# Kernel tuning notes

Measured on AMD Instinct MI355X. Metric: run time of the kernel, lower is better.

## Reference

```python
import jax, jax.numpy as jnp
import numpy as np

L = 12      # n_layers
C = 768     # n_embd = dim = dim_att
H = 12      # heads
N = 64      # head_size_a
FF = 2688   # dim_ffn = int(768*3.5//32*32)
P = 2       # patch_size
INCH = 4
IMG = 32
NCLS = 1000
FREQ = 256
HC = C // 2  # conv stem channels (dim//2)
B = 32
D_MIX = 32
D_DEC = 64
LNX_EPS = 1e-5 * 8.0 ** 2  # GroupNorm eps with head_size_divisor=8


def _ln(x, w=None, b=None, eps=1e-5):
    m = x.mean(-1, keepdims=True)
    v = x.var(-1, keepdims=True)
    xh = (x - m) * jax.lax.rsqrt(v + eps)
    if w is not None:
        xh = xh * w + b
    return xh


def _shift(x):  # RWKV token shift: prepend zero row, drop last
    return jnp.pad(x, ((0, 0), (1, 0), (0, 0)))[:, :-1]


def _gn_img(x, w, b, groups=32, eps=1e-5):
    Bb, Ch, Hh, Ww = x.shape
    xg = x.reshape(Bb, groups, Ch // groups, Hh, Ww)
    m = xg.mean((2, 3, 4), keepdims=True)
    v = xg.var((2, 3, 4), keepdims=True)
    xg = (xg - m) * jax.lax.rsqrt(v + eps)
    return xg.reshape(Bb, Ch, Hh, Ww) * w[None, :, None, None] + b[None, :, None, None]


def _conv5(x, w, b):
    y = jax.lax.conv_general_dilated(x, w, (1, 1), ((2, 2), (2, 2)),
                                     dimension_numbers=('NCHW', 'OIHW', 'NCHW'))
    return y + b[None, :, None, None]


def _wkv(r, k, v, w, u):
    # r,k,v,w: (B,T,H,N); u: (H,N). S[b,h,i,j]: key i -> value j.
    def step(S, inp):
        rt, kt, vt, wt = inp  # each (B,H,N)
        kv = kt[..., :, None] * vt[..., None, :]           # (B,H,N,N)
        y = jnp.einsum('bhi,bhij->bhj', rt, S + u[None, :, :, None] * kv)
        S = wt[..., :, None] * S + kv
        return S, y
    S0 = jnp.zeros((r.shape[0], H, N, N), r.dtype)
    seq = tuple(jnp.moveaxis(a, 1, 0) for a in (r, k, v, w))
    _, ys = jax.lax.scan(step, S0, seq)
    return jnp.moveaxis(ys, 0, 1)  # (B,T,H,N)


def _timemix(x, p):
    Bb, Tt, _ = x.shape
    xx = _shift(x) - x
    xxx = x + xx * p['maa'][0]
    mix = jnp.tanh(xxx @ p['tm_w1']).reshape(Bb, Tt, 5, D_MIX)
    m = jnp.einsum('btfd,fdc->fbtc', mix, p['tm_w2'])  # (5,B,T,C): mw,mk,mv,mr,mg
    xw = x + xx * (p['maa'][1] + m[0])
    xk = x + xx * (p['maa'][2] + m[1])
    xv = x + xx * (p['maa'][3] + m[2])
    xr = x + xx * (p['maa'][4] + m[3])
    xg = x + xx * (p['maa'][5] + m[4])
    r = (xr @ p['r_w'].T).reshape(Bb, Tt, H, N)
    k = (xk @ p['k_w'].T).reshape(Bb, Tt, H, N)
    v = (xv @ p['v_w'].T).reshape(Bb, Tt, H, N)
    g = jax.nn.silu(xg @ p['g_w'].T)
    ww = p['td'] + jnp.tanh(xw @ p['td_w1']) @ p['td_w2']
    w = jnp.exp(-jnp.exp(ww)).reshape(Bb, Tt, H, N)
    y = _wkv(r, k, v, w, p['faaaa'])  # (B,T,H,N)
    mn = y.mean(-1, keepdims=True)
    vr = y.var(-1, keepdims=True)
    y = ((y - mn) * jax.lax.rsqrt(vr + LNX_EPS)).reshape(Bb, Tt, C) * p['lnx_w'] + p['lnx_b']
    return (y * g) @ p['o_w'].T


def _chanmix(x, p):
    xx = _shift(x) - x
    xk = x + xx * p['fmaa'][0]
    xr = x + xx * p['fmaa'][1]
    k = jnp.square(jax.nn.relu(xk @ p['fk_w'].T))
    return jax.nn.sigmoid(xr @ p['fr_w'].T) * (k @ p['fv_w'].T)


def _forward(x, t, y, c1_w, c1_b, gn1_w, gn1_b, c2_w, c2_b, gn2_w, gn2_b,
             xe_w, xe_b, te_w1, te_b1, te_w2, te_b2, y_tab, ln0_w, ln0_b,
             ln1_w, ln1_b, ln2_w, ln2_b, att_maa, tm_w1, tm_w2, td, td_w1,
             td_w2, faaaa, r_w, k_w, v_w, o_w, g_w, lnx_w, lnx_b, ffn_maa,
             fk_w, fr_w, fv_w, ada_w, ada_b, fl_ada_w, fl_ada_b, fl_w, fl_b):
    Bb = x.shape[0]
    h = jax.nn.silu(_conv5(x, c1_w, c1_b))
    h = _gn_img(h, gn1_w, gn1_b)
    h = jax.nn.silu(_conv5(h, c2_w, c2_b))
    h = _gn_img(h, gn2_w, gn2_b)
    # patchify: (B,HC,IMG,IMG) -> (B,T,P*P*HC)
    G = IMG // P
    h = h.reshape(Bb, HC, G, P, G, P).transpose(0, 2, 4, 1, 3, 5).reshape(Bb, G * G, HC * P * P)
    xs = h @ xe_w.T + xe_b
    # timestep embedding
    half = FREQ // 2
    freqs = jnp.exp(-jnp.log(10000.0) * jnp.arange(half, dtype=jnp.float32) / half)
    ang = t[:, None] * freqs[None]
    temb = jnp.concatenate([jnp.cos(ang), jnp.sin(ang)], -1)
    temb = jax.nn.silu(temb @ te_w1.T + te_b1) @ te_w2.T + te_b2
    c = temb + y_tab[y]  # adaln_input (B,C)
    for l in range(L):
        ada = jax.nn.silu(c) @ ada_w[l].T + ada_b[l]
        sm, scm, gm, sp, scp, gp = jnp.split(ada, 6, axis=1)
        if l == 0:
            xs = _ln(xs, ln0_w, ln0_b)
        p = dict(maa=att_maa[l], tm_w1=tm_w1[l], tm_w2=tm_w2[l], td=td[l],
                 td_w1=td_w1[l], td_w2=td_w2[l], faaaa=faaaa[l], r_w=r_w[l],
                 k_w=k_w[l], v_w=v_w[l], o_w=o_w[l], g_w=g_w[l], lnx_w=lnx_w[l],
                 lnx_b=lnx_b[l], fmaa=ffn_maa[l], fk_w=fk_w[l], fr_w=fr_w[l],
                 fv_w=fv_w[l])
        hmod = _ln(xs, ln1_w[l], ln1_b[l]) * (1 + scm[:, None, :]) + sm[:, None, :]
        xs = xs + gm[:, None, :] * _timemix(hmod, p)
        hmod = _ln(xs, ln2_w[l], ln2_b[l]) * (1 + scp[:, None, :]) + sp[:, None, :]
        xs = xs + gp[:, None, :] * _chanmix(hmod, p)
    ada = jax.nn.silu(c) @ fl_ada_w.T + fl_ada_b
    sh, sc = jnp.split(ada, 2, axis=1)
    out = (_ln(xs, eps=1e-6) * (1 + sc[:, None, :]) + sh[:, None, :]) @ fl_w.T + fl_b
    G = IMG // P
    out = out.reshape(Bb, G, G, P, P, INCH)
    out = jnp.einsum('nhwpqc->nchpwq', out).reshape(Bb, INCH, IMG, IMG)
    return out


def setup_inputs() -> dict:
    key = jax.random.key(0)
    ks = iter(jax.random.split(key, 64))
    def rn(shape, s=0.02):
        return (jax.random.normal(next(ks), shape) * s).astype(jnp.float32)
    inp = {}
    inp['x'] = jax.random.normal(next(ks), (B, INCH, IMG, IMG), jnp.float32)
    inp['t'] = jax.random.uniform(next(ks), (B,), jnp.float32) * 1000.0
    inp['y'] = jax.random.randint(next(ks), (B,), 0, NCLS)
    inp['c1_w'] = rn((HC, INCH, 5, 5), 0.05); inp['c1_b'] = jnp.zeros(HC)
    inp['gn1_w'] = jnp.ones(HC); inp['gn1_b'] = jnp.zeros(HC)
    inp['c2_w'] = rn((HC, HC, 5, 5), 0.02); inp['c2_b'] = jnp.zeros(HC)
    inp['gn2_w'] = jnp.ones(HC); inp['gn2_b'] = jnp.zeros(HC)
    inp['xe_w'] = rn((C, P * P * HC)); inp['xe_b'] = jnp.zeros(C)
    inp['te_w1'] = rn((C, FREQ)); inp['te_b1'] = jnp.zeros(C)
    inp['te_w2'] = rn((C, C)); inp['te_b2'] = jnp.zeros(C)
    inp['y_tab'] = rn((NCLS + 1, C))
    inp['ln0_w'] = jnp.ones(C); inp['ln0_b'] = jnp.zeros(C)
    inp['ln1_w'] = jnp.ones((L, C)); inp['ln1_b'] = jnp.zeros((L, C))
    inp['ln2_w'] = jnp.ones((L, C)); inp['ln2_b'] = jnp.zeros((L, C))
    inp['att_maa'] = jax.random.uniform(next(ks), (L, 6, C), jnp.float32)
    inp['tm_w1'] = rn((L, C, 5 * D_MIX), 0.01)
    inp['tm_w2'] = rn((L, 5, D_MIX, C), 0.01)
    inp['td'] = rn((L, C), 0.5) - 3.0
    inp['td_w1'] = rn((L, C, D_DEC), 0.01)
    inp['td_w2'] = rn((L, D_DEC, C), 0.01)
    inp['faaaa'] = rn((L, H, N), 0.1)
    for nm in ('r_w', 'k_w', 'v_w', 'o_w', 'g_w'):
        inp[nm] = rn((L, C, C))
    inp['lnx_w'] = jnp.ones((L, C)); inp['lnx_b'] = jnp.zeros((L, C))
    inp['ffn_maa'] = jax.random.uniform(next(ks), (L, 2, C), jnp.float32)
    inp['fk_w'] = rn((L, FF, C)); inp['fr_w'] = rn((L, C, C)); inp['fv_w'] = rn((L, C, FF))
    inp['ada_w'] = rn((L, 6 * C, C)); inp['ada_b'] = jnp.zeros((L, 6 * C))
    inp['fl_ada_w'] = rn((2 * C, C)); inp['fl_ada_b'] = jnp.zeros(2 * C)
    inp['fl_w'] = rn((P * P * INCH, C)); inp['fl_b'] = jnp.zeros(P * P * INCH)
    return inp


def reference(x, t, y, c1_w, c1_b, gn1_w, gn1_b, c2_w, c2_b, gn2_w, gn2_b,
              xe_w, xe_b, te_w1, te_b1, te_w2, te_b2, y_tab, ln0_w, ln0_b,
              ln1_w, ln1_b, ln2_w, ln2_b, att_maa, tm_w1, tm_w2, td, td_w1,
              td_w2, faaaa, r_w, k_w, v_w, o_w, g_w, lnx_w, lnx_b, ffn_maa,
              fk_w, fr_w, fv_w, ada_w, ada_b, fl_ada_w, fl_ada_b, fl_w, fl_b):
    return _forward(x, t, y, c1_w, c1_b, gn1_w, gn1_b, c2_w, c2_b, gn2_w, gn2_b,
                    xe_w, xe_b, te_w1, te_b1, te_w2, te_b2, y_tab, ln0_w, ln0_b,
                    ln1_w, ln1_b, ln2_w, ln2_b, att_maa, tm_w1, tm_w2, td, td_w1,
                    td_w2, faaaa, r_w, k_w, v_w, o_w, g_w, lnx_w, lnx_b, ffn_maa,
                    fk_w, fr_w, fv_w, ada_w, ada_b, fl_ada_w, fl_ada_b, fl_w, fl_b)
```

## Files before the change

### kernel.cpp

```cpp
#include <hip/hip_runtime.h>
#include <math.h>


typedef short  s16x8 __attribute__((ext_vector_type(8)));
typedef float  f32x4 __attribute__((ext_vector_type(4)));
typedef __attribute__((address_space(1))) const void as1_cv;
typedef __attribute__((address_space(3))) void as3_v;

#define GLDS16(gp, lp) __builtin_amdgcn_global_load_lds( \
    (as1_cv*)(unsigned long long)(const void*)(gp), \
    (as3_v*)(unsigned int)(unsigned long long)(void*)(lp), 16, 0, 0)

static __device__ __forceinline__ float sigf(float x){ return 1.f/(1.f+expf(-x)); }
static __device__ __forceinline__ unsigned short f2b(float x){
  unsigned int u = __builtin_bit_cast(unsigned int, x);
  unsigned int r = (u + 0x7FFFu + ((u >> 16) & 1u)) >> 16;
  return (unsigned short)r;
}
static __device__ __forceinline__ float b2f(unsigned short h){
  unsigned int u = ((unsigned int)h)<<16; return __builtin_bit_cast(float,u);
}

static const size_t O_XS    = 0ull;
static const size_t O_HMOD  = 6291456ull;
static const size_t O_ADA   = 12582912ull;
static const size_t O_FLA   = 14352384ull;
static const size_t O_T2    = 14401536ull;
static const size_t O_SC    = 14426112ull;
static const size_t O_TI    = 14450688ull;
static const size_t O_T1    = 14458880ull;
static const size_t O_ST1   = 14483456ull;
static const size_t O_ST2   = 14485504ull;
static const size_t O_XEW16 = 14487552ull;
static const size_t O_WL16  = 15077376ull;
static const size_t O_BIG   = 19107840ull;
static const size_t L_XW    = 0ull;
static const size_t L_XX    = 6291456ull;
static const size_t L_XXX   = 12582912ull;
static const size_t L_KB    = 18874368ull;
static const size_t L_VB    = 25165824ull;
static const size_t L_GB    = 31457280ull;
static const size_t L_WD    = 37748736ull;
static const size_t L_MIXB  = 50331648ull;
static const size_t L_WT    = 51642368ull;
static const size_t L_XK16  = 52166656ull;
static const size_t L_XV16  = 55312384ull;
static const size_t L_XR16  = 58458112ull;
static const size_t L_XG16  = 61603840ull;
static const size_t L_GNH16 = 64749568ull;
static const size_t L_KBIG16= 67895296ull;
static const size_t S_IMG1  = 0ull;
static const size_t S_IMG2  = 12582912ull;
static const size_t S_PAD16 = 25165824ull;
static const size_t S_WTAP16= 33128448ull;
static const size_t S_PM16  = 34971648ull;

enum { EPI_NONE=0, EPI_SILU=1 };

template<int EPI, bool TB>
__global__ __launch_bounds__(256) void gemm_k(
    const float* __restrict__ A, const float* __restrict__ B,
    float* __restrict__ C, const float* __restrict__ bias,
    int M, int N, int K)
{
  __shared__ __align__(16) float As[16][68];
  __shared__ __align__(16) float Bs[16][68];
  const int tid = threadIdx.x;
  const int tx = tid & 15, ty = tid >> 4;
  const int row0 = blockIdx.y * 64, col0 = blockIdx.x * 64;
  const int lr = tid >> 2;
  const int lk = (tid & 3) << 2;
  float acc[4][4] = {};
  for (int k0 = 0; k0 < K; k0 += 16) {
    {
      int gr = row0 + lr;
      float4 v = make_float4(0.f,0.f,0.f,0.f);
      if (gr < M) v = *reinterpret_cast<const float4*>(A + (size_t)gr*K + (k0 + lk));
      As[lk+0][lr]=v.x; As[lk+1][lr]=v.y; As[lk+2][lr]=v.z; As[lk+3][lr]=v.w;
    }
    if (TB) {
      int gr = col0 + lr;
      float4 v = make_float4(0.f,0.f,0.f,0.f);
      if (gr < N) v = *reinterpret_cast<const float4*>(B + (size_t)gr*K + (k0 + lk));
      Bs[lk+0][lr]=v.x; Bs[lk+1][lr]=v.y; Bs[lk+2][lr]=v.z; Bs[lk+3][lr]=v.w;
    } else {
      int kr = tid >> 4;
      int gc = col0 + ((tid & 15) << 2);
      float4 v = make_float4(0.f,0.f,0.f,0.f);
      if (gc < N) v = *reinterpret_cast<const float4*>(B + (size_t)(k0+kr)*N + gc);
      Bs[kr][((tid&15)<<2)+0]=v.x; Bs[kr][((tid&15)<<2)+1]=v.y;
      Bs[kr][((tid&15)<<2)+2]=v.z; Bs[kr][((tid&15)<<2)+3]=v.w;
    }
    __syncthreads();
    #pragma unroll
    for (int kk=0;kk<16;kk++){
      const float4 a4 = *reinterpret_cast<const float4*>(&As[kk][ty<<2]);
      const float4 b4 = *reinterpret_cast<const float4*>(&Bs[kk][tx<<2]);
      const float av[4]={a4.x,a4.y,a4.z,a4.w};
      const float bv[4]={b4.x,b4.y,b4.z,b4.w};
      #pragma unroll
      for (int i=0;i<4;i++)
        #pragma unroll
        for (int j=0;j<4;j++)
          acc[i][j]=fmaf(av[i],bv[j],acc[i][j]);
    }
    __syncthreads();
  }
  #pragma unroll
  for (int i=0;i<4;i++){
    const int r = row0 + (ty<<2) + i;
    if (r >= M) break;
    #pragma unroll
    for (int j=0;j<4;j++){
      const int c = col0 + (tx<<2) + j;
      if (c >= N) break;
      float v = acc[i][j];
      if (bias) v += bias[c];
      const size_t idx = (size_t)r*N + c;
      if (EPI==EPI_NONE)        C[idx]=v;
      else if (EPI==EPI_SILU)   C[idx]=v*sigf(v);
    }
  }
}

#define GEMM(EPI,TB,A,B,C,bias,M,N,K) \
  gemm_k<EPI,TB><<<dim3(((N)+63)/64,((M)+63)/64),dim3(256),0,stream>>>((A),(B),(C),(bias),(M),(N),(K))

enum { BEPI_F32=0, BEPI_BIAS_F32, BEPI_SILU_F32, BEPI_SIG_F32, BEPI_RELU2_BF16,
       BEPI_RES_GM, BEPI_RES_GP16, BEPI_TANH_BF16, BEPI_WDEC_F32 };

template<int EPI>
__global__ __launch_bounds__(256) void bgemm_k(
    const unsigned short* __restrict__ A, const unsigned short* __restrict__ B,
    void* __restrict__ Cv, const float* __restrict__ bias,
    const float* __restrict__ p1, const void* __restrict__ p2, int pstride,
    int M, int N, int K)
{
  __shared__ __align__(16) unsigned short As[128][64];
  __shared__ __align__(16) unsigned short Bs[128][64];
  const int tid = threadIdx.x;
  const int w = tid >> 6, lane = tid & 63;
  const int row0 = blockIdx.y * 128, col0 = blockIdx.x * 128;
  const int wr = w >> 1, wc = w & 1;
  const int l15 = lane & 15, l4 = lane >> 4;
  const int kkc = ((lane & 7) ^ (lane >> 3)) * 8;
  f32x4 acc[4][4] = {};
  for (int k0 = 0; k0 < K; k0 += 64) {
    #pragma unroll
    for (int i = 0; i < 4; i++) {
      const int rb = i*32 + w*8;
      const int r  = rb + (lane >> 3);
      GLDS16(A + (size_t)(row0 + r)*K + k0 + kkc, &As[rb][0]);
      GLDS16(B + (size_t)(col0 + r)*K + k0 + kkc, &Bs[rb][0]);
    }
    __syncthreads();
    #pragma unroll
    for (int ks = 0; ks < 2; ks++) {
      s16x8 af[4], bf[4];
      #pragma unroll
      for (int m = 0; m < 4; m++) {
        const int r = wr*64 + m*16 + l15;
        const int sl = (ks*4 + l4) ^ (r & 7);
        af[m] = *reinterpret_cast<const s16x8*>(&As[r][sl*8]);
      }
      #pragma unroll
      for (int n = 0; n < 4; n++) {
        const int r = wc*64 + n*16 + l15;
        const int sl = (ks*4 + l4) ^ (r & 7);
        bf[n] = *reinterpret_cast<const s16x8*>(&Bs[r][sl*8]);
      }
      #pragma unroll
      for (int m = 0; m < 4; m++)
        #pragma unroll
        for (int n = 0; n < 4; n++)
          acc[m][n] = __builtin_amdgcn_mfma_f32_16x16x32_bf16(af[m], bf[n], acc[m][n], 0, 0, 0);
    }
    __syncthreads();
  }
  float* Cf = (float*)Cv; unsigned short* Ch = (unsigned short*)Cv;
  const unsigned short* p2h = (const unsigned short*)p2;
  #pragma unroll
  for (int m = 0; m < 4; m++) {
    const int rbase = row0 + wr*64 + m*16 + (l4<<2);
    #pragma unroll
    for (int n = 0; n < 4; n++) {
      const int c = col0 + wc*64 + n*16 + l15;
      if (c >= N) continue;
      #pragma unroll
      for (int q = 0; q < 4; q++) {
        const int r = rbase + q;
        const int bb = r >> 8;
        float v = acc[m][n][q];
        const size_t idx = (size_t)r*N + c;
        if (EPI==BEPI_F32)            Cf[idx] = v;
        else if (EPI==BEPI_BIAS_F32)  Cf[idx] = v + bias[c];
        else if (EPI==BEPI_SILU_F32)  Cf[idx] = v*sigf(v);
        else if (EPI==BEPI_SIG_F32)   Cf[idx] = sigf(v);
        else if (EPI==BEPI_RELU2_BF16){ float t=fmaxf(v,0.f); Ch[idx] = f2b(t*t); }
        else if (EPI==BEPI_RES_GM)    Cf[idx] += p1[(size_t)bb*pstride + c]*v;
        else if (EPI==BEPI_RES_GP16)  Cf[idx] += p1[(size_t)bb*pstride + c]*(b2f(p2h[idx])*v);
        else if (EPI==BEPI_TANH_BF16) Ch[idx] = f2b(tanhf(v));
        else if (EPI==BEPI_WDEC_F32)  Cf[idx] = expf(-expf(v + p1[c]));
      }
    }
  }
}

#define BGEMM(EPI,A16,B16,Cp,bias,p1,p2,ps,M,N,K) \
  bgemm_k<EPI><<<dim3(((N)+127)/128,(M)/128),dim3(256),0,stream>>>( \
    (const unsigned short*)(A16),(const unsigned short*)(B16),(void*)(Cp),(bias),(p1),(p2),(ps),(M),(N),(K))

struct BGrp { const unsigned short* A; const unsigned short* B; void* C;
              int epi; int N; int gx; };
struct BGrp4 { BGrp g[4]; };

__global__ __launch_bounds__(256) void bgemm_grp_k(BGrp4 G, int M, int K)
{
  const BGrp gr = G.g[blockIdx.z];
  if ((int)blockIdx.x >= gr.gx) return;
  __shared__ __align__(16) unsigned short As[128][64];
  __shared__ __align__(16) unsigned short Bs[128][64];
  const int tid = threadIdx.x;
  const int w = tid >> 6, lane = tid & 63;
  const int row0 = blockIdx.y * 128, col0 = blockIdx.x * 128;
  const int wr = w >> 1, wc = w & 1;
  const int l15 = lane & 15, l4 = lane >> 4;
  const int kkc = ((lane & 7) ^ (lane >> 3)) * 8;
  const int N = gr.N;
  f32x4 acc[4][4] = {};
  for (int k0 = 0; k0 < K; k0 += 64) {
    #pragma unroll
    for (int i = 0; i < 4; i++) {
      const int rb = i*32 + w*8;
      const int r  = rb + (lane >> 3);
      GLDS16(gr.A + (size_t)(row0 + r)*K + k0 + kkc, &As[rb][0]);
      GLDS16(gr.B + (size_t)(col0 + r)*K + k0 + kkc, &Bs[rb][0]);
    }
    __syncthreads();
    #pragma unroll
    for (int ks = 0; ks < 2; ks++) {
      s16x8 af[4], bf[4];
      #pragma unroll
      for (int m = 0; m < 4; m++) {
        const int r = wr*64 + m*16 + l15;
        const int sl = (ks*4 + l4) ^ (r & 7);
        af[m] = *reinterpret_cast<const s16x8*>(&As[r][sl*8]);
      }
      #pragma unroll
      for (int n = 0; n < 4; n++) {
        const int r = wc*64 + n*16 + l15;
        const int sl = (ks*4 + l4) ^ (r & 7);
        bf[n] = *reinterpret_cast<const s16x8*>(&Bs[r][sl*8]);
      }
      #pragma unroll
      for (int m = 0; m < 4; m++)
        #pragma unroll
        for (int n = 0; n < 4; n++)
          acc[m][n] = __builtin_amdgcn_mfma_f32_16x16x32_bf16(af[m], bf[n], acc[m][n], 0, 0, 0);
    }
    __syncthreads();
  }
  float* Cf = (float*)gr.C; unsigned short* Ch = (unsigned short*)gr.C;
  #pragma unroll
  for (int m = 0; m < 4; m++) {
    const int rbase = row0 + wr*64 + m*16 + (l4<<2);
    #pragma unroll
    for (int n = 0; n < 4; n++) {
      const int c = col0 + wc*64 + n*16 + l15;
      #pragma unroll
      for (int q = 0; q < 4; q++) {
        const int r = rbase + q;
        float v = acc[m][n][q];
        const size_t idx = (size_t)r*N + c;
        switch (gr.epi) {
          case 0: Cf[idx] = v; break;
          case 1: Cf[idx] = v*sigf(v); break;
          case 3: { float t=fmaxf(v,0.f); Ch[idx] = f2b(t*t); } break;
          case 4: Ch[idx] = f2b(v); break;
          case 5: Ch[idx] = f2b(v*sigf(v)); break;
          default: Ch[idx] = f2b(sigf(v)); break;
        }
      }
    }
  }
}

__global__ __launch_bounds__(256) void conv1_k(
    const float* __restrict__ x, const float* __restrict__ w,
    const float* __restrict__ bias, float* __restrict__ out)
{
  const int blk = blockIdx.x; const int bb = blk / 384; const int oc = blk % 384;
  __shared__ __align__(16) float sIn[4*1296];
  __shared__ __align__(16) float sW[100];
  const int tid = threadIdx.x;
  for (int idx=tid; idx<4*1296; idx+=256){
    int ic = idx/1296; int rem = idx - ic*1296;
    int yy = rem/36, xx = rem - yy*36;
    int gy = yy-2, gx = xx-2;
    float v = 0.f;
    if ((unsigned)gy < 32u && (unsigned)gx < 32u)
      v = x[(((size_t)bb*4+ic)*32+gy)*32+gx];
    sIn[idx]=v;
  }
  if (tid < 100) sW[tid] = w[(size_t)oc*100 + tid];
  __syncthreads();
  const float bv = bias[oc];
  #pragma unroll
  for (int i=0;i<4;i++){
    int p = tid + 256*i; int py=p>>5, px=p&31;
    int pb = py*36+px;
    float acc = bv;
    #pragma unroll
    for (int ic=0;ic<4;ic++)
      #pragma unroll
      for (int ky=0;ky<5;ky++)
        #pragma unroll
        for (int kx=0;kx<5;kx++)
          acc = fmaf(sIn[ic*1296 + pb + ky*36+kx], sW[ic*25+ky*5+kx], acc);
    out[((size_t)(bb*384+oc))*1024 + p] = acc*sigf(acc);
  }
}

__global__ __launch_bounds__(256) void gn_stats_nchw_k(
    const float* __restrict__ h, float* __restrict__ stats)
{
  const int blk = blockIdx.x;
  const size_t base = (size_t)blk*12288;
  const int tid = threadIdx.x;
  float s=0.f, s2=0.f;
  for (int idx=tid; idx<12288; idx+=256){ float v=h[base+idx]; s+=v; s2=fmaf(v,v,s2); }
  #pragma unroll
  for (int mask=32; mask>=1; mask>>=1){ s += __shfl_xor(s,mask); s2 += __shfl_xor(s2,mask); }
// ... 257 lines not shown
    const float d = pv - h;
    hmod16[base+c] = f2b(h);
    xx16[base+c] = f2b(d);
    xxx16[base+c] = f2b(fmaf(d, maa0[c], h));
  }
}

__global__ __launch_bounds__(256) void ln_shift_cm_k(
    const float* __restrict__ xs, const float* __restrict__ w, const float* __restrict__ b,
    const float* __restrict__ mod, const float* __restrict__ fmaa,
    unsigned short* __restrict__ xk16, unsigned short* __restrict__ xr16)
{
  const int m = blockIdx.x, tid = threadIdx.x;
  const size_t base = (size_t)m*768;
  const int t = m & 255, bb = m >> 8;
  float c0=xs[base+tid], c1=xs[base+tid+256], c2=xs[base+tid+512];
  float p0=0.f,p1=0.f,p2=0.f;
  if (t) { p0=xs[base-768+tid]; p1=xs[base-512+tid]; p2=xs[base-256+tid]; }
  float sc_=c0+c1+c2, sc2=fmaf(c0,c0,fmaf(c1,c1,c2*c2));
  float sp_=p0+p1+p2, sp2=fmaf(p0,p0,fmaf(p1,p1,p2*p2));
  #pragma unroll
  for (int mask=32; mask>=1; mask>>=1){
    sc_+=__shfl_xor(sc_,mask); sc2+=__shfl_xor(sc2,mask);
    sp_+=__shfl_xor(sp_,mask); sp2+=__shfl_xor(sp2,mask);
  }
  __shared__ float ps[16];
  if ((tid&63)==0){ int wv=tid>>6; ps[wv]=sc_; ps[4+wv]=sc2; ps[8+wv]=sp_; ps[12+wv]=sp2; }
  __syncthreads();
  sc_=ps[0]+ps[1]+ps[2]+ps[3]; sc2=ps[4]+ps[5]+ps[6]+ps[7];
  sp_=ps[8]+ps[9]+ps[10]+ps[11]; sp2=ps[12]+ps[13]+ps[14]+ps[15];
  const float mc = sc_*(1.f/768.f), rc = rsqrtf(sc2*(1.f/768.f)-mc*mc + 1e-5f);
  const float mp = sp_*(1.f/768.f), rp = rsqrtf(sp2*(1.f/768.f)-mp*mp + 1e-5f);
  #pragma unroll
  for (int k=0;k<3;k++){
    const int c = tid + k*256;
    const float scv = mod[(size_t)bb*55296 + 3072 + c];
    const float shv = mod[(size_t)bb*55296 + 2304 + c];
    float cv = (k==0)?c0:((k==1)?c1:c2);
    float h = fmaf((cv-mc)*rc, w[c], b[c]);
    h = fmaf(h, 1.f+scv, shv);
    float pv = 0.f;
    if (t) {
      float pk = (k==0)?p0:((k==1)?p1:p2);
      pv = fmaf((pk-mp)*rp, w[c], b[c]);
      pv = fmaf(pv, 1.f+scv, shv);
    }
    const float d = pv - h;
    xk16[base+c] = f2b(fmaf(d, fmaa[c], h));
    xr16[base+c] = f2b(fmaf(d, fmaa[768+c], h));
  }
}

__global__ __launch_bounds__(256) void five_mix_k(
    const unsigned short* __restrict__ mix16, const float* __restrict__ w2,
    const unsigned short* __restrict__ hmod16, const unsigned short* __restrict__ xx16,
    const float* __restrict__ maa15,
    unsigned short* __restrict__ xw, unsigned short* __restrict__ xk,
    unsigned short* __restrict__ xv, unsigned short* __restrict__ xr,
    unsigned short* __restrict__ xg)
{
  __shared__ __align__(16) float smix[16][160];
  const int m0 = blockIdx.x * 16;
  const int tid = threadIdx.x;
  for (int idx=tid; idx<16*160; idx+=256){
    int r = idx/160, d = idx - r*160;
    smix[r][d] = b2f(mix16[(size_t)(m0+r)*160 + d]);
  }
  __syncthreads();
  #pragma unroll 1
  for (int cc=0; cc<3; cc++){
    const int c = tid + cc*256;
    float hv[16], xv_[16];
    #pragma unroll
    for (int r=0;r<16;r++){
      size_t id=(size_t)(m0+r)*768+c;
      hv[r]=b2f(hmod16[id]); xv_[r]=b2f(xx16[id]);
    }
    #pragma unroll 1
    for (int f=0; f<5; f++){
      float acc[16];
      const float base = maa15[f*768 + c];
      #pragma unroll
      for (int r=0;r<16;r++) acc[r]=base;
      #pragma unroll 1
      for (int d4=0; d4<8; d4++){
        float wv[4];
        #pragma unroll
        for (int q=0;q<4;q++) wv[q] = w2[(size_t)(f*32+d4*4+q)*768 + c];
        #pragma unroll
        for (int r=0;r<16;r++){
          const float4 mv = *reinterpret_cast<const float4*>(&smix[r][f*32+d4*4]);
          acc[r] = fmaf(mv.x,wv[0],fmaf(mv.y,wv[1],fmaf(mv.z,wv[2],fmaf(mv.w,wv[3],acc[r]))));
        }
      }
      #pragma unroll
      for (int r=0;r<16;r++){
        float val = fmaf(xv_[r], acc[r], hv[r]);
        size_t id = (size_t)(m0+r)*768+c;
        if (f==0) xw[id]=f2b(val);
        else if (f==1) xk[id]=f2b(val);
        else if (f==2) xv[id]=f2b(val);
        else if (f==3) xr[id]=f2b(val);
        else           xg[id]=f2b(val);
      }
    }
  }
}

__global__ __launch_bounds__(256) void wkv_k(
    const unsigned short* __restrict__ rg, const unsigned short* __restrict__ kg,
    const unsigned short* __restrict__ vg, const float* __restrict__ wg,
    const unsigned short* __restrict__ gg, const float* __restrict__ u,
    const float* __restrict__ lnxw, const float* __restrict__ lnxb,
    unsigned short* __restrict__ out16)
{
  const int bh = blockIdx.x; const int b = bh/12, h = bh%12;
  const int tid = threadIdx.x;
  const int w = tid >> 6, lane = tid & 63;
  const int l4 = lane >> 4, l15 = lane & 15;
  __shared__ __align__(16) unsigned short r16s[32][64], k16s[32][64], v16s[32][64], g16s[32][64];
  __shared__ __align__(16) float wds[32][64];
  __shared__ __align__(16) float Wl[33][64];
  __shared__ __align__(16) unsigned short rr16[32][64], kk16[32][64];
  __shared__ __align__(16) unsigned short kk2T[64][32], vT[64][32];
  __shared__ __align__(16) unsigned short S16T[64][64];
  __shared__ __align__(16) unsigned short A16[32][32];
  __shared__ float diag[32], ypsum[32][4], ypsq[32][4];

  reinterpret_cast<uint4*>(&S16T[0][0])[tid] = make_uint4(0,0,0,0);
  reinterpret_cast<uint4*>(&S16T[0][0])[256+tid] = make_uint4(0,0,0,0);

  const float u_lane = u[h*64 + lane];
  const int jj = w*16 + l15;
  const float lw = lnxw[h*64 + jj], lb = lnxb[h*64 + jj];
  const size_t gb = (size_t)(b*256)*768 + h*64;

  const int st_t = tid >> 3, st_i = (tid & 7) * 8;
  uint4 pr, pk, pv, pg; float4 pw0, pw1;

#define WKV_LOADC(c_) { \
    const size_t tb = gb + (size_t)((c_)*32 + st_t)*768 + st_i; \
    pr = *reinterpret_cast<const uint4*>(rg + tb); \
    pk = *reinterpret_cast<const uint4*>(kg + tb); \
    pv = *reinterpret_cast<const uint4*>(vg + tb); \
    pg = *reinterpret_cast<const uint4*>(gg + tb); \
    pw0 = *reinterpret_cast<const float4*>(wg + tb); \
    pw1 = *reinterpret_cast<const float4*>(wg + tb + 4); }
#define WKV_STAGE() { \
    *reinterpret_cast<uint4*>(&r16s[st_t][st_i]) = pr; \
    *reinterpret_cast<uint4*>(&k16s[st_t][st_i]) = pk; \
    *reinterpret_cast<uint4*>(&v16s[st_t][st_i]) = pv; \
    *reinterpret_cast<uint4*>(&g16s[st_t][st_i]) = pg; \
    *reinterpret_cast<float4*>(&wds[st_t][st_i]) = pw0; \
    *reinterpret_cast<float4*>(&wds[st_t][st_i+4]) = pw1; }

  f32x4 S_acc[4] = {};

  WKV_LOADC(0);
  WKV_STAGE();
  __syncthreads();

  #pragma unroll 1
  for (int c = 0; c < 8; ++c) {
    if (w == 0) {
      float wv[32];
      #pragma unroll
      for (int t=0;t<32;t++) wv[t] = wds[t][lane];
      float P = 1.f;
      Wl[0][lane] = 1.f;
      #pragma unroll
      for (int t=0;t<32;t++){ P *= wv[t]; Wl[t+1][lane] = P; }
    }
    __syncthreads();
    {
      const int t = st_t, i0 = st_i;
      s16x8 rv = *reinterpret_cast<const s16x8*>(&r16s[t][i0]);
      s16x8 kv = *reinterpret_cast<const s16x8*>(&k16s[t][i0]);
      s16x8 vv = *reinterpret_cast<const s16x8*>(&v16s[t][i0]);
      float4 wa0 = *reinterpret_cast<const float4*>(&Wl[t][i0]);
      float4 wa1 = *reinterpret_cast<const float4*>(&Wl[t][i0+4]);
      float4 wb0 = *reinterpret_cast<const float4*>(&Wl[t+1][i0]);
      float4 wb1 = *reinterpret_cast<const float4*>(&Wl[t+1][i0+4]);
      float4 wf0 = *reinterpret_cast<const float4*>(&Wl[32][i0]);
      float4 wf1 = *reinterpret_cast<const float4*>(&Wl[32][i0+4]);
      float wt_[8] = {wa0.x,wa0.y,wa0.z,wa0.w,wa1.x,wa1.y,wa1.z,wa1.w};
      float wt1[8] = {wb0.x,wb0.y,wb0.z,wb0.w,wb1.x,wb1.y,wb1.z,wb1.w};
      float w32[8] = {wf0.x,wf0.y,wf0.z,wf0.w,wf1.x,wf1.y,wf1.z,wf1.w};
      s16x8 rro, kko;
      #pragma unroll
      for (int e=0;e<8;e++){
        const int i = i0 + e;
        float rf = b2f((unsigned short)rv[e]) * wt_[e];
        float kf = b2f((unsigned short)kv[e]) / wt1[e];
        rro[e] = (short)f2b(rf);
        kko[e] = (short)f2b(kf);
        kk2T[i][(((t>>3)^(i&3))<<3) + (t&7)] = f2b(kf * w32[e]);
        vT[i][(((t>>3)^(i&3))<<3) + (t&7)] = (unsigned short)vv[e];
      }
      const int sc_ = ((i0>>3)^(t&7))<<3;
      *reinterpret_cast<s16x8*>(&rr16[t][sc_]) = rro;
      *reinterpret_cast<s16x8*>(&kk16[t][sc_]) = kko;
      #pragma unroll
      for (int tt=0;tt<8;tt++){
        const int td = w*8 + tt;
        float p = b2f(r16s[td][lane]) * u_lane * b2f(k16s[td][lane]);
        #pragma unroll
        for (int mask=32; mask>=1; mask>>=1) p += __shfl_xor(p, mask);
        if (lane==0) diag[td] = p;
      }
    }
    __syncthreads();
    if (c < 7) WKV_LOADC(c+1);
    f32x4 Y[2] = {};
    s16x8 rrf[2][2];
    #pragma unroll
    for (int m=0;m<2;m++)
// ... 64 lines not shown
        float s1 = Y[m][q], s2 = s1*s1;
        #pragma unroll
        for (int mask=8; mask>=1; mask>>=1){ s1 += __shfl_xor(s1,mask); s2 += __shfl_xor(s2,mask); }
        if (l15==0){ const int t = m*16 + l4*4 + q; ypsum[t][w]=s1; ypsq[t][w]=s2; }
      }
    __syncthreads();
    #pragma unroll
    for (int m=0;m<2;m++)
      #pragma unroll
      for (int q=0;q<4;q++){
        const int t = m*16 + l4*4 + q;
        float s1 = ypsum[t][0]+ypsum[t][1]+ypsum[t][2]+ypsum[t][3];
        float s2 = ypsq[t][0]+ypsq[t][1]+ypsq[t][2]+ypsq[t][3];
        float mean = s1*(1.f/64.f);
        float var  = s2*(1.f/64.f) - mean*mean;
        float xh = (Y[m][q]-mean)*rsqrtf(var + 6.4e-4f);
        float o = fmaf(xh, lw, lb) * b2f(g16s[t][jj]);
        out16[gb + (size_t)(c*32+t)*768 + jj] = f2b(o);
      }
    if (c < 7) {
      __syncthreads();
      WKV_STAGE();
      __syncthreads();
    }
  }
#undef WKV_LOADC
#undef WKV_STAGE
}

__global__ void unpatch_k(const float* __restrict__ po, float* __restrict__ out)
{
  int idx = blockIdx.x*256 + threadIdx.x;
  int xq=idx&31; int yy=(idx>>5)&31; int ch=(idx>>10)&3; int bb=idx>>12;
  int gh=yy>>1, p=yy&1, gw=xq>>1, q=xq&1;
  out[idx] = po[((size_t)(bb*256+gh*16+gw))*16 + p*8+q*4+ch];
}

__global__ void f2b_k(const float* __restrict__ s, unsigned short* __restrict__ d)
{
  size_t i = ((size_t)blockIdx.x*256 + threadIdx.x)*8;
  float4 a = *reinterpret_cast<const float4*>(s+i);
  float4 b = *reinterpret_cast<const float4*>(s+i+4);
  s16x8 o;
  o[0]=(short)f2b(a.x); o[1]=(short)f2b(a.y); o[2]=(short)f2b(a.z); o[3]=(short)f2b(a.w);
  o[4]=(short)f2b(b.x); o[5]=(short)f2b(b.y); o[6]=(short)f2b(b.z); o[7]=(short)f2b(b.w);
  *reinterpret_cast<s16x8*>(d + i) = o;
}

__global__ void f2bw_layer_k(
    const float* __restrict__ r_, const float* __restrict__ k_, const float* __restrict__ v_,
    const float* __restrict__ o_, const float* __restrict__ g_, const float* __restrict__ fr_,
    const float* __restrict__ fk_, const float* __restrict__ fv_,
    const float* __restrict__ tm1, const float* __restrict__ td1, const float* __restrict__ td2,
    unsigned short* __restrict__ dst)
{
  if (blockIdx.x < 3744) {
    size_t i = ((size_t)blockIdx.x*256 + threadIdx.x)*8;
    const float* s; size_t off;
    if (i < 3538944) {
      unsigned seg = (unsigned)(i / 589824u); off = i - (size_t)seg*589824u;
      s = seg==0?r_:seg==1?k_:seg==2?v_:seg==3?o_:seg==4?g_:fr_;
    } else if (i < 5603328) { s = fk_; off = i - 3538944; }
    else                    { s = fv_; off = i - 5603328; }
    float4 a = *reinterpret_cast<const float4*>(s+off);
    float4 b = *reinterpret_cast<const float4*>(s+off+4);
    s16x8 o;
    o[0]=(short)f2b(a.x); o[1]=(short)f2b(a.y); o[2]=(short)f2b(a.z); o[3]=(short)f2b(a.w);
    o[4]=(short)f2b(b.x); o[5]=(short)f2b(b.y); o[6]=(short)f2b(b.z); o[7]=(short)f2b(b.w);
    *reinterpret_cast<s16x8*>(dst + i) = o;
  } else {
    int idx = (blockIdx.x-3744)*256 + threadIdx.x;
    unsigned short* rp = dst + 7667712;
    if (idx < 196608) {
      int n = idx/768, k = idx - n*768;
      rp[idx] = (n<160) ? f2b(tm1[(size_t)k*160 + n]) : (unsigned short)0;
    } else if (idx < 294912) {
      int i = idx-196608; int n = i/768, k = i - n*768;
      rp[idx] = (n<64) ? f2b(td1[(size_t)k*64 + n]) : (unsigned short)0;
    } else {
      int i = idx-294912; int n = i/64, k = i - n*64;
      rp[idx] = f2b(td2[(size_t)k*768 + n]);
    }
  }
}

extern "C" void kernel_launch(void* const* d_in, const int* in_sizes, int n_in,
                              void* d_out, int out_size, void* d_ws, size_t ws_size,
                              hipStream_t stream)
{
  const float* x_in  = (const float*)d_in[0];
  const float* t_in  = (const float*)d_in[1];
  const int*   y_in  = (const int*)  d_in[2];
  const float* c1w   = (const float*)d_in[3];
  const float* c1b   = (const float*)d_in[4];
  const float* gn1w  = (const float*)d_in[5];
  const float* gn1b  = (const float*)d_in[6];
  const float* c2w   = (const float*)d_in[7];
  const float* c2b   = (const float*)d_in[8];
  const float* gn2w  = (const float*)d_in[9];
  const float* gn2b  = (const float*)d_in[10];
  const float* xew   = (const float*)d_in[11];
  const float* xeb   = (const float*)d_in[12];
  const float* tew1  = (const float*)d_in[13];
  const float* teb1  = (const float*)d_in[14];
  const float* tew2  = (const float*)d_in[15];
  const float* teb2  = (const float*)d_in[16];
  const float* ytab  = (const float*)d_in[17];
  const float* ln0w  = (const float*)d_in[18];
  const float* ln0b  = (const float*)d_in[19];
  const float* ln1w  = (const float*)d_in[20];
  const float* ln1b  = (const float*)d_in[21];
  const float* ln2w  = (const float*)d_in[22];
  const float* ln2b  = (const float*)d_in[23];
  const float* amaa  = (const float*)d_in[24];
  const float* tmw1  = (const float*)d_in[25];
  const float* tmw2  = (const float*)d_in[26];
  const float* tdv   = (const float*)d_in[27];
  const float* tdw1  = (const float*)d_in[28];
  const float* tdw2  = (const float*)d_in[29];
  const float* faa   = (const float*)d_in[30];
  const float* rw    = (const float*)d_in[31];
  const float* kw    = (const float*)d_in[32];
  const float* vw    = (const float*)d_in[33];
  const float* ow    = (const float*)d_in[34];
  const float* gw    = (const float*)d_in[35];
  const float* lnxw  = (const float*)d_in[36];
  const float* lnxb  = (const float*)d_in[37];
  const float* fmaa  = (const float*)d_in[38];
  const float* fkw   = (const float*)d_in[39];
  const float* frw   = (const float*)d_in[40];
  const float* fvw   = (const float*)d_in[41];
  const float* adaw  = (const float*)d_in[42];
  const float* adab  = (const float*)d_in[43];
  const float* flaw  = (const float*)d_in[44];
  const float* flab  = (const float*)d_in[45];
  const float* flw   = (const float*)d_in[46];
  const float* flb   = (const float*)d_in[47];

  float* Wf = (float*)d_ws;
  float* xs   = Wf+O_XS;   float* hmodf = Wf+O_HMOD;
  float* ada  = Wf+O_ADA;  float* fla  = Wf+O_FLA;
  float* t2   = Wf+O_T2;   float* sc   = Wf+O_SC;
  float* ti   = Wf+O_TI;   float* t1   = Wf+O_T1;
  float* st1  = Wf+O_ST1;  float* st2  = Wf+O_ST2;
  unsigned short* xew16 = (unsigned short*)(Wf+O_XEW16);
  unsigned short* wl16  = (unsigned short*)(Wf+O_WL16);
  unsigned short* hmod16 = (unsigned short*)(Wf+O_HMOD);
  float* big = Wf+O_BIG;
  float* wd   = big+L_WD;
  unsigned short* xx16  = (unsigned short*)(big+L_XX);
  unsigned short* rb16  = (unsigned short*)(big+L_XXX);
  unsigned short* kb16  = (unsigned short*)(big+L_KB);
  unsigned short* vb16  = (unsigned short*)(big+L_VB);
  unsigned short* gb16  = (unsigned short*)(big+L_GB);
  unsigned short* xw16  = (unsigned short*)(big+L_XW);
  unsigned short* xxx16 = (unsigned short*)(big+L_XXX);
  unsigned short* mixb16= (unsigned short*)(big+L_MIXB);
  unsigned short* wt16  = (unsigned short*)(big+L_WT);
  unsigned short* xk16 = (unsigned short*)(big+L_XK16);
  unsigned short* xv16 = (unsigned short*)(big+L_XV16);
  unsigned short* xr16 = (unsigned short*)(big+L_XR16);
  unsigned short* xg16 = (unsigned short*)(big+L_XG16);
  unsigned short* gnh16 = (unsigned short*)(big+L_GNH16);
  unsigned short* kbig16 = (unsigned short*)(big+L_KBIG16);
  float* img1 = big+S_IMG1;
  unsigned short* img2_16 = (unsigned short*)(big+S_IMG2);
  unsigned short* pad16  = (unsigned short*)(big+S_PAD16);
  unsigned short* wtap16 = (unsigned short*)(big+S_WTAP16);
  unsigned short* pm16   = (unsigned short*)(big+S_PM16);
  float* pout = big+L_MIXB;
  unsigned short* dr  = wl16;
  unsigned short* dk  = wl16 + 589824;
  unsigned short* dv  = wl16 + 1179648;
  unsigned short* do_ = wl16 + 1769472;
  unsigned short* dg  = wl16 + 2359296;
  unsigned short* dfr = wl16 + 2949120;
  unsigned short* dfk = wl16 + 3538944;
  unsigned short* dfv = wl16 + 5603328;
  unsigned short* dtm1t = wl16 + 7667712;
  unsigned short* dtd1t = wl16 + 7864320;
  unsigned short* dtd2t = wl16 + 7962624;

  conv1_k<<<dim3(32*384),dim3(256),0,stream>>>(x_in, c1w, c1b, img1);
  gn_stats_nchw_k<<<dim3(1024),dim3(256),0,stream>>>(img1, st1);
  zero16_k<<<dim3(7776),dim3(256),0,stream>>>(pad16);
  pad_apply_k<<<dim3(1024),dim3(256),0,stream>>>(img1, st1, gn1w, gn1b, pad16);
  wrepack_k<<<dim3(384),dim3(256),0,stream>>>(c2w, wtap16);
  conv2m_k<<<dim3(768),dim3(256),0,stream>>>(pad16, wtap16, c2b, img2_16);
  gn_stats_nhwc_k<<<dim3(1024),dim3(256),0,stream>>>(img2_16, st2);
  patchify_gn_k<<<dim3(49152),dim3(256),0,stream>>>(img2_16, st2, gn2w, gn2b, pm16);
  f2b_k<<<dim3(576),dim3(256),0,stream>>>(xew, xew16);
  BGEMM(BEPI_BIAS_F32, pm16, xew16, xs, xeb, nullptr,nullptr,0, 8192,768,1536);

  temb_in_k<<<dim3(32),dim3(128),0,stream>>>(t_in, ti);
  GEMM(EPI_SILU,true, ti, tew1, t1, teb1, 32,768,256);
  GEMM(EPI_NONE,true, t1, tew2, t2, teb2, 32,768,768);
  siluc_k<<<dim3(32),dim3(256),0,stream>>>(t2, ytab, y_in, sc);
  GEMM(EPI_NONE,true, sc, adaw, ada, adab, 32,55296,768);
  GEMM(EPI_NONE,true, sc, flaw, fla, flab, 32,1536,768);

  ln_mod_k<<<dim3(8192),dim3(256),0,stream>>>(xs, xs, ln0w, ln0b, nullptr, 0,0,0, 1e-5f);

  for (int l=0; l<12; l++){
    const float* adal = ada + (size_t)l*4608;
    f2bw_layer_k<<<dim3(5088),dim3(256),0,stream>>>(
        rw+(size_t)l*589824, kw+(size_t)l*589824, vw+(size_t)l*589824,
        ow+(size_t)l*589824, gw+(size_t)l*589824, frw+(size_t)l*589824,
        fkw+(size_t)l*2064384, fvw+(size_t)l*2064384,
        tmw1+(size_t)l*122880, tdw1+(size_t)l*49152, tdw2+(size_t)l*49152, wl16);
    ln_shift_tm_k<<<dim3(8192),dim3(256),0,stream>>>(
        xs, ln1w+(size_t)l*768, ln1b+(size_t)l*768, adal, amaa+(size_t)l*4608,
        hmod16, xx16, xxx16);
    BGEMM(BEPI_TANH_BF16, xxx16, dtm1t, mixb16, nullptr,nullptr,nullptr,0, 8192,160,768);
    five_mix_k<<<dim3(512),dim3(256),0,stream>>>(mixb16, tmw2+(size_t)l*122880, hmod16, xx16,
                                                 amaa+(size_t)l*4608+768, xw16,xk16,xv16,xr16,xg16);
    BGEMM(BEPI_TANH_BF16, xw16, dtd1t, wt16, nullptr,nullptr,nullptr,0, 8192,64,768);
    BGEMM(BEPI_WDEC_F32, wt16, dtd2t, wd, nullptr, tdv+(size_t)l*768, nullptr,0, 8192,768,64);
    {
      BGrp4 G;
      G.g[0].A=xr16; G.g[0].B=dr; G.g[0].C=rb16; G.g[0].epi=4; G.g[0].N=768; G.g[0].gx=6;
      G.g[1].A=xk16; G.g[1].B=dk; G.g[1].C=kb16; G.g[1].epi=4; G.g[1].N=768; G.g[1].gx=6;
      G.g[2].A=xv16; G.g[2].B=dv; G.g[2].C=vb16; G.g[2].epi=4; G.g[2].N=768; G.g[2].gx=6;
      G.g[3].A=xg16; G.g[3].B=dg; G.g[3].C=gb16; G.g[3].epi=5; G.g[3].N=768; G.g[3].gx=6;
      bgemm_grp_k<<<dim3(6,64,4),dim3(256),0,stream>>>(G, 8192, 768);
    }
    wkv_k<<<dim3(384),dim3(256),0,stream>>>(rb16, kb16, vb16, wd, gb16, faa+(size_t)l*768,
                                            lnxw+(size_t)l*768, lnxb+(size_t)l*768, gnh16);
    BGEMM(BEPI_RES_GM, gnh16, do_, xs, nullptr, adal+1536, nullptr, 55296, 8192,768,768);
    ln_shift_cm_k<<<dim3(8192),dim3(256),0,stream>>>(
        xs, ln2w+(size_t)l*768, ln2b+(size_t)l*768, adal, fmaa+(size_t)l*1536, xk16, xr16);
    {
      BGrp4 G;
      G.g[0].A=xk16; G.g[0].B=dfk; G.g[0].C=kbig16; G.g[0].epi=3; G.g[0].N=2688; G.g[0].gx=21;
      G.g[1].A=xr16; G.g[1].B=dfr; G.g[1].C=gb16;   G.g[1].epi=7; G.g[1].N=768;  G.g[1].gx=6;
      G.g[2]=G.g[1]; G.g[3]=G.g[1];
      bgemm_grp_k<<<dim3(21,64,2),dim3(256),0,stream>>>(G, 8192, 768);
    }
    BGEMM(BEPI_RES_GP16, kbig16, dfv, xs, nullptr, adal+3840, gb16, 55296, 8192,768,2688);
  }

  ln_mod_k<<<dim3(8192),dim3(256),0,stream>>>(xs, hmodf, nullptr, nullptr, fla, 1536, 0, 768, 1e-6f);
  GEMM(EPI_NONE,true, hmodf, flw, pout, flb, 8192,16,768);
  unpatch_k<<<dim3(512),dim3(256),0,stream>>>(pout, (float*)d_out);
}
```

Before: 8.233 ms.

## Fuse decay LoRA into grouped GEMM and WKV kernel, bf16 tm_w2

The first decay-LoRA projection (xw @ td_w1, tanh) becomes a fifth group in the grouped r/k/v/g GEMM launch. The second projection plus the exp(-exp) decay is now computed per chunk inside the WKV kernel with MFMA, so the fp32 8192x768 decay tensor is no longer written to and re-read from global memory. tm_w2 is also converted to bf16 in the per-layer weight conversion kernel, halving its reads in five_mix. The trade-off is extra compute and a new __syncthreads per chunk in the serial WKV kernel, plus slightly lower precision for the mix weights.

New measurement: 9.152 ms. 11.2% more time.

```diff
diff --git a/kernel.cpp b/kernel.cpp
--- a/kernel.cpp
+++ b/kernel.cpp
@@ -33,7 +33,7 @@
 static const size_t O_ST2   = 14485504ull;
 static const size_t O_XEW16 = 14487552ull;
 static const size_t O_WL16  = 15077376ull;
-static const size_t O_BIG   = 19107840ull;
+static const size_t O_BIG   = 19144704ull;
 static const size_t L_XW    = 0ull;
 static const size_t L_XX    = 6291456ull;
 static const size_t L_XXX   = 12582912ull;
@@ -127,7 +127,7 @@
   gemm_k<EPI,TB><<<dim3(((N)+63)/64,((M)+63)/64),dim3(256),0,stream>>>((A),(B),(C),(bias),(M),(N),(K))
 
 enum { BEPI_F32=0, BEPI_BIAS_F32, BEPI_SILU_F32, BEPI_SIG_F32, BEPI_RELU2_BF16,
-       BEPI_RES_GM, BEPI_RES_GP16, BEPI_TANH_BF16, BEPI_WDEC_F32 };
+       BEPI_RES_GM, BEPI_RES_GP16, BEPI_TANH_BF16 };
 
 template<int EPI>
 __global__ __launch_bounds__(256) void bgemm_k(
@@ -200,7 +200,6 @@
         else if (EPI==BEPI_RES_GM)    Cf[idx] += p1[(size_t)bb*pstride + c]*v;
         else if (EPI==BEPI_RES_GP16)  Cf[idx] += p1[(size_t)bb*pstride + c]*(b2f(p2h[idx])*v);
         else if (EPI==BEPI_TANH_BF16) Ch[idx] = f2b(tanhf(v));
-        else if (EPI==BEPI_WDEC_F32)  Cf[idx] = expf(-expf(v + p1[c]));
       }
     }
   }
@@ -212,9 +211,9 @@
 
 struct BGrp { const unsigned short* A; const unsigned short* B; void* C;
               int epi; int N; int gx; };
-struct BGrp4 { BGrp g[4]; };
-
-__global__ __launch_bounds__(256) void bgemm_grp_k(BGrp4 G, int M, int K)
+struct BGrp5 { BGrp g[5]; };
+
+__global__ __launch_bounds__(256) void bgemm_grp_k(BGrp5 G, int M, int K)
 {
   const BGrp gr = G.g[blockIdx.z];
   if ((int)blockIdx.x >= gr.gx) return;
@@ -267,6 +266,7 @@
     #pragma unroll
     for (int n = 0; n < 4; n++) {
       const int c = col0 + wc*64 + n*16 + l15;
+      if (c >= N) continue;
       #pragma unroll
       for (int q = 0; q < 4; q++) {
         const int r = rbase + q;
@@ -278,6 +278,7 @@
           case 3: { float t=fmaxf(v,0.f); Ch[idx] = f2b(t*t); } break;
           case 4: Ch[idx] = f2b(v); break;
           case 5: Ch[idx] = f2b(v*sigf(v)); break;
+          case 6: Ch[idx] = f2b(tanhf(v)); break;
           default: Ch[idx] = f2b(sigf(v)); break;
         }
       }
@@ -641,7 +642,7 @@
 }
 
 __global__ __launch_bounds__(256) void five_mix_k(
-    const unsigned short* __restrict__ mix16, const float* __restrict__ w2,
+    const unsigned short* __restrict__ mix16, const unsigned short* __restrict__ w2,
     const unsigned short* __restrict__ hmod16, const unsigned short* __restrict__ xx16,
     const float* __restrict__ maa15,
     unsigned short* __restrict__ xw, unsigned short* __restrict__ xk,
@@ -675,7 +676,7 @@
       for (int d4=0; d4<8; d4++){
         float wv[4];
         #pragma unroll
-        for (int q=0;q<4;q++) wv[q] = w2[(size_t)(f*32+d4*4+q)*768 + c];
+        for (int q=0;q<4;q++) wv[q] = b2f(w2[(size_t)(f*32+d4*4+q)*768 + c]);
         #pragma unroll
         for (int r=0;r<16;r++){
           const float4 mv = *reinterpret_cast<const float4*>(&smix[r][f*32+d4*4]);
@@ -698,8 +699,9 @@
 
 __global__ __launch_bounds__(256) void wkv_k(
     const unsigned short* __restrict__ rg, const unsigned short* __restrict__ kg,
-    const unsigned short* __restrict__ vg, const float* __restrict__ wg,
-    const unsigned short* __restrict__ gg, const float* __restrict__ u,
+    const unsigned short* __restrict__ vg, const unsigned short* __restrict__ gg,
+    const unsigned short* __restrict__ wtp, const unsigned short* __restrict__ td2w,
+    const float* __restrict__ tdvp, const float* __restrict__ u,
     const float* __restrict__ lnxw, const float* __restrict__ lnxb,
     unsigned short* __restrict__ out16)
 {
@@ -724,24 +726,27 @@
   const float lw = lnxw[h*64 + jj], lb = lnxb[h*64 + jj];
   const size_t gb = (size_t)(b*256)*768 + h*64;
 
+  s16x8 wdb[2];
+  #pragma unroll
+  for (int ks=0; ks<2; ks++)
+    wdb[ks] = *reinterpret_cast<const s16x8*>(td2w + (size_t)(h*64 + jj)*64 + (ks*4+l4)*8);
+  const float tdv_r = tdvp[h*64 + jj];
+  const size_t wtbase = (size_t)(b*256)*64;
+
   const int st_t = tid >> 3, st_i = (tid & 7) * 8;
-  uint4 pr, pk, pv, pg; float4 pw0, pw1;
+  uint4 pr, pk, pv, pg;
 
 #define WKV_LOADC(c_) { \
     const size_t tb = gb + (size_t)((c_)*32 + st_t)*768 + st_i; \
     pr = *reinterpret_cast<const uint4*>(rg + tb); \
     pk = *reinterpret_cast<const uint4*>(kg + tb); \
     pv = *reinterpret_cast<const uint4*>(vg + tb); \
-    pg = *reinterpret_cast<const uint4*>(gg + tb); \
-    pw0 = *reinterpret_cast<const float4*>(wg + tb); \
-    pw1 = *reinterpret_cast<const float4*>(wg + tb + 4); }
+    pg = *reinterpret_cast<const uint4*>(gg + tb); }
 #define WKV_STAGE() { \
     *reinterpret_cast<uint4*>(&r16s[st_t][st_i]) = pr; \
     *reinterpret_cast<uint4*>(&k16s[st_t][st_i]) = pk; \
     *reinterpret_cast<uint4*>(&v16s[st_t][st_i]) = pv; \
-    *reinterpret_cast<uint4*>(&g16s[st_t][st_i]) = pg; \
-    *reinterpret_cast<float4*>(&wds[st_t][st_i]) = pw0; \
-    *reinterpret_cast<float4*>(&wds[st_t][st_i+4]) = pw1; }
+    *reinterpret_cast<uint4*>(&g16s[st_t][st_i]) = pg; }
 
   f32x4 S_acc[4] = {};
 
@@ -751,6 +756,23 @@
 
   #pragma unroll 1
   for (int c = 0; c < 8; ++c) {
+    {
+      f32x4 wdacc[2] = {};
+      #pragma unroll
+      for (int m=0;m<2;m++)
+        #pragma unroll
+        for (int ks=0;ks<2;ks++){
+          s16x8 wa = *reinterpret_cast<const s16x8*>(
+              wtp + wtbase + (size_t)(c*32 + m*16 + l15)*64 + (ks*4+l4)*8);
+          wdacc[m] = __builtin_amdgcn_mfma_f32_16x16x32_bf16(wa, wdb[ks], wdacc[m], 0,0,0);
+        }
+      #pragma unroll
+      for (int m=0;m<2;m++)
+        #pragma unroll
+        for (int q=0;q<4;q++)
+          wds[m*16 + l4*4 + q][jj] = expf(-expf(wdacc[m][q] + tdv_r));
+    }
+    __syncthreads();
     if (w == 0) {
       float wv[32];
       #pragma unroll
@@ -921,7 +943,7 @@
     const float* __restrict__ o_, const float* __restrict__ g_, const float* __restrict__ fr_,
     const float* __restrict__ fk_, const float* __restrict__ fv_,
     const float* __restrict__ tm1, const float* __restrict__ td1, const float* __restrict__ td2,
-    unsigned short* __restrict__ dst)
+    const float* __restrict__ tm2, unsigned short* __restrict__ dst)
 {
   if (blockIdx.x < 3744) {
     size_t i = ((size_t)blockIdx.x*256 + threadIdx.x)*8;
@@ -946,9 +968,12 @@
     } else if (idx < 294912) {
       int i = idx-196608; int n = i/768, k = i - n*768;
       rp[idx] = (n<64) ? f2b(td1[(size_t)k*64 + n]) : (unsigned short)0;
-    } else {
+    } else if (idx < 344064) {
       int i = idx-294912; int n = i/64, k = i - n*64;
       rp[idx] = f2b(td2[(size_t)k*768 + n]);
+    } else {
+      int i = idx-344064;
+      rp[idx] = f2b(tm2[i]);
     }
   }
 }
@@ -1016,7 +1041,6 @@
   unsigned short* wl16  = (unsigned short*)(Wf+O_WL16);
   unsigned short* hmod16 = (unsigned short*)(Wf+O_HMOD);
   float* big = Wf+O_BIG;
-  float* wd   = big+L_WD;
   unsigned short* xx16  = (unsigned short*)(big+L_XX);
   unsigned short* rb16  = (unsigned short*)(big+L_XXX);
   unsigned short* kb16  = (unsigned short*)(big+L_KB);
@@ -1049,6 +1073,7 @@
   unsigned short* dtm1t = wl16 + 7667712;
   unsigned short* dtd1t = wl16 + 7864320;
   unsigned short* dtd2t = wl16 + 7962624;
+  unsigned short* dtmw2 = wl16 + 8011776;
 
   conv1_k<<<dim3(32*384),dim3(256),0,stream>>>(x_in, c1w, c1b, img1);
   gn_stats_nchw_k<<<dim3(1024),dim3(256),0,stream>>>(img1, st1);
@@ -1072,37 +1097,38 @@
 
   for (int l=0; l<12; l++){
     const float* adal = ada + (size_t)l*4608;
-    f2bw_layer_k<<<dim3(5088),dim3(256),0,stream>>>(
+    f2bw_layer_k<<<dim3(5568),dim3(256),0,stream>>>(
         rw+(size_t)l*589824, kw+(size_t)l*589824, vw+(size_t)l*589824,
         ow+(size_t)l*589824, gw+(size_t)l*589824, frw+(size_t)l*589824,
         fkw+(size_t)l*2064384, fvw+(size_t)l*2064384,
-        tmw1+(size_t)l*122880, tdw1+(size_t)l*49152, tdw2+(size_t)l*49152, wl16);
+        tmw1+(size_t)l*122880, tdw1+(size_t)l*49152, tdw2+(size_t)l*49152,
+        tmw2+(size_t)l*122880, wl16);
     ln_shift_tm_k<<<dim3(8192),dim3(256),0,stream>>>(
         xs, ln1w+(size_t)l*768, ln1b+(size_t)l*768, adal, amaa+(size_t)l*4608,
         hmod16, xx16, xxx16);
     BGEMM(BEPI_TANH_BF16, xxx16, dtm1t, mixb16, nullptr,nullptr,nullptr,0, 8192,160,768);
-    five_mix_k<<<dim3(512),dim3(256),0,stream>>>(mixb16, tmw2+(size_t)l*122880, hmod16, xx16,
+    five_mix_k<<<dim3(512),dim3(256),0,stream>>>(mixb16, dtmw2, hmod16, xx16,
                                                  amaa+(size_t)l*4608+768, xw16,xk16,xv16,xr16,xg16);
-    BGEMM(BEPI_TANH_BF16, xw16, dtd1t, wt16, nullptr,nullptr,nullptr,0, 8192,64,768);
-    BGEMM(BEPI_WDEC_F32, wt16, dtd2t, wd, nullptr, tdv+(size_t)l*768, nullptr,0, 8192,768,64);
     {
-      BGrp4 G;
-      G.g[0].A=xr16; G.g[0].B=dr; G.g[0].C=rb16; G.g[0].epi=4; G.g[0].N=768; G.g[0].gx=6;
-      G.g[1].A=xk16; G.g[1].B=dk; G.g[1].C=kb16; G.g[1].epi=4; G.g[1].N=768; G.g[1].gx=6;
-      G.g[2].A=xv16; G.g[2].B=dv; G.g[2].C=vb16; G.g[2].epi=4; G.g[2].N=768; G.g[2].gx=6;
-      G.g[3].A=xg16; G.g[3].B=dg; G.g[3].C=gb16; G.g[3].epi=5; G.g[3].N=768; G.g[3].gx=6;
-      bgemm_grp_k<<<dim3(6,64,4),dim3(256),0,stream>>>(G, 8192, 768);
-    }
-    wkv_k<<<dim3(384),dim3(256),0,stream>>>(rb16, kb16, vb16, wd, gb16, faa+(size_t)l*768,
+      BGrp5 G;
+      G.g[0].A=xr16; G.g[0].B=dr;    G.g[0].C=rb16; G.g[0].epi=4; G.g[0].N=768; G.g[0].gx=6;
+      G.g[1].A=xk16; G.g[1].B=dk;    G.g[1].C=kb16; G.g[1].epi=4; G.g[1].N=768; G.g[1].gx=6;
+      G.g[2].A=xv16; G.g[2].B=dv;    G.g[2].C=vb16; G.g[2].epi=4; G.g[2].N=768; G.g[2].gx=6;
+      G.g[3].A=xg16; G.g[3].B=dg;    G.g[3].C=gb16; G.g[3].epi=5; G.g[3].N=768; G.g[3].gx=6;
+      G.g[4].A=xw16; G.g[4].B=dtd1t; G.g[4].C=wt16; G.g[4].epi=6; G.g[4].N=64;  G.g[4].gx=1;
+      bgemm_grp_k<<<dim3(6,64,5),dim3(256),0,stream>>>(G, 8192, 768);
+    }
+    wkv_k<<<dim3(384),dim3(256),0,stream>>>(rb16, kb16, vb16, gb16, wt16, dtd2t,
+                                            tdv+(size_t)l*768, faa+(size_t)l*768,
                                             lnxw+(size_t)l*768, lnxb+(size_t)l*768, gnh16);
     BGEMM(BEPI_RES_GM, gnh16, do_, xs, nullptr, adal+1536, nullptr, 55296, 8192,768,768);
     ln_shift_cm_k<<<dim3(8192),dim3(256),0,stream>>>(
         xs, ln2w+(size_t)l*768, ln2b+(size_t)l*768, adal, fmaa+(size_t)l*1536, xk16, xr16);
     {
-      BGrp4 G;
+      BGrp5 G;
       G.g[0].A=xk16; G.g[0].B=dfk; G.g[0].C=kbig16; G.g[0].epi=3; G.g[0].N=2688; G.g[0].gx=21;
       G.g[1].A=xr16; G.g[1].B=dfr; G.g[1].C=gb16;   G.g[1].epi=7; G.g[1].N=768;  G.g[1].gx=6;
-      G.g[2]=G.g[1]; G.g[3]=G.g[1];
+      G.g[2]=G.g[1]; G.g[3]=G.g[1]; G.g[4]=G.g[1];
       bgemm_grp_k<<<dim3(21,64,2),dim3(256),0,stream>>>(G, 8192, 768);
     }
     BGEMM(BEPI_RES_GP16, kbig16, dfv, xs, nullptr, adal+3840, gb16, 55296, 8192,768,2688);
```
